# Kernel optimization log

Hardware: AMD Instinct MI355X
Metric: run time of the kernel (lower is better)

The kernel has to match this reference:

```python
import jax, jax.numpy as jnp
import numpy as np

BATCH = 8192
IN_FEATURES = 64
K = 10
OUT_FEATURES = 1000  # classifier assumed fully expanded: t == out_features
SCALING = 1.0
EPS = 1e-12  # F.normalize default eps


def _l2_normalize(v, axis):
    n = jnp.sqrt(jnp.sum(v * v, axis=axis, keepdims=True))
    return v / jnp.maximum(n, EPS)


def setup_inputs() -> dict:
    key = jax.random.key(0)
    k1, k2 = jax.random.split(key)
    x = jax.random.normal(k1, (BATCH, IN_FEATURES), dtype=jnp.float32)
    # kaiming_uniform_(a=sqrt(5)) on (in_features, k, out_features): fan_in = k*out_features
    fan_in = K * OUT_FEATURES
    bound = np.sqrt(6.0 / ((1.0 + 5.0) * fan_in))
    theta = jax.random.uniform(k2, (IN_FEATURES, K, OUT_FEATURES), dtype=jnp.float32,
                               minval=-bound, maxval=bound)
    return {"x": x, "theta": theta}


def reference(x, theta):
    d, k, C = theta.shape
    # theta.permute(0,2,1).reshape(d, C*k).T -> rows are class-major, then proxy index
    th = jnp.transpose(theta, (0, 2, 1)).reshape(d, C * k).T  # (C*k, d)
    th = SCALING * _l2_normalize(th, axis=1)
    a = SCALING * _l2_normalize(x, axis=1)  # (B, d)
    # Only the cross a-theta block of the full pairwise matrix is used downstream;
    # the eye/off-diagonal mask never intersects it (row i < B <= col B+j).
    d2 = (jnp.sum(a * a, axis=1, keepdims=True)
          + jnp.sum(th * th, axis=1)[None, :]
          - 2.0 * (a @ th.T))  # (B, C*k)
    d2 = jnp.maximum(d2, 0.0)
    d2 = jnp.where(d2 > 0.0, d2, 0.0)  # error_mask zeroing (no-op after clamp, kept for fidelity)
    simi = -d2.reshape(x.shape[0], C, k)  # (B, C, k)
    att = jax.nn.softmax(simi, axis=-1)  # gamma = 1
    return jnp.sum(simi * att, axis=-1)  # (B, C)
```

## Files before the change

### kernel.cpp

```cpp
#include <hip/hip_runtime.h>


#define BATCH   8192
#define DIM     64
#define KPROX   10
#define NCLASS  1000
#define NCOL    (NCLASS * KPROX)
#define NBTILE  (BATCH / 16)
#define NNTILE  (NCOL / 16)

#define NBM     32
#define NBN     63
#define XBLKS   (NBTILE / 4)
#define TBLKS   ((NCOL + 255) / 256)

typedef __attribute__((ext_vector_type(8))) short bf16x8;
typedef __attribute__((ext_vector_type(4))) float f32x4;
typedef __attribute__((ext_vector_type(2))) unsigned int u32x2;
typedef __attribute__((ext_vector_type(2))) __fp16 f16x2;
typedef __attribute__((ext_vector_type(4))) __fp16 f16x4;

#define LOG2E 1.4426950408889634f
#define LN2   0.6931471805599453f

__device__ inline unsigned short f32_to_bf16(float f) {
    unsigned int u = __float_as_uint(f);
    u += 0x7FFFu + ((u >> 16) & 1u);
    return (unsigned short)(u >> 16);
}

__device__ inline bf16x8 gload16(const unsigned short* p) {
    bf16x8 r;
    asm volatile("global_load_dwordx4 %0, %1, off" : "=v"(r) : "v"(p));
    return r;
}
__device__ inline float fexp2(float x) {
    float r; asm("v_exp_f32 %0, %1" : "=v"(r) : "v"(x)); return r;
}
#define WAIT_VM(N) do { asm volatile("s_waitcnt vmcnt(" #N ")" ::: "memory"); \
                        __builtin_amdgcn_sched_barrier(0); } while (0)

__global__ __launch_bounds__(256)
void prep_kernel(const float* __restrict__ x, const float* __restrict__ theta,
                 unsigned short* __restrict__ Xf0, unsigned short* __restrict__ Xf1,
                 unsigned short* __restrict__ THf0, unsigned short* __restrict__ THf1) {
    if (blockIdx.x < XBLKS) {
        int wave = threadIdx.x >> 6, lane = threadIdx.x & 63;
        int bt  = blockIdx.x * 4 + wave;
        int r16 = lane & 15, hi = lane >> 4;
        const float* src = x + (size_t)(bt * 16 + r16) * DIM + hi * 8;
        f32x4 v0 = *(const f32x4*)(src);
        f32x4 v1 = *(const f32x4*)(src + 4);
        f32x4 v2 = *(const f32x4*)(src + 32);
        f32x4 v3 = *(const f32x4*)(src + 36);
        float ss = 0.f;
        #pragma unroll
        for (int i = 0; i < 4; ++i)
            ss += v0[i]*v0[i] + v1[i]*v1[i] + v2[i]*v2[i] + v3[i]*v3[i];
        ss += __shfl_xor(ss, 16);
        ss += __shfl_xor(ss, 32);
        float sc = __builtin_amdgcn_rsqf(ss);
        bf16x8 p0, p1;
        #pragma unroll
        for (int i = 0; i < 4; ++i) {
            p0[i]     = (short)f32_to_bf16(v0[i] * sc);
            p0[i + 4] = (short)f32_to_bf16(v1[i] * sc);
            p1[i]     = (short)f32_to_bf16(v2[i] * sc);
            p1[i + 4] = (short)f32_to_bf16(v3[i] * sc);
        }
        ((bf16x8*)Xf0)[bt * 64 + lane] = p0;
        ((bf16x8*)Xf1)[bt * 64 + lane] = p1;
    } else {
        int tid = (blockIdx.x - XBLKS) * 256 + threadIdx.x;
        if (tid >= NCOL) return;
        int kk = tid / NCLASS, c = tid - kk * NCLASS;
        const float* src = theta + kk * NCLASS + c;
        float v[DIM];
        float ss = 0.f;
        #pragma unroll
        for (int d = 0; d < DIM; ++d) {
            v[d] = src[(size_t)d * NCOL];
            ss += v[d] * v[d];
        }
        float sc = __builtin_amdgcn_rsqf(ss);
        int j = c * KPROX + kk;
        int jt = j >> 4, jr = j & 15;
        #pragma unroll
        for (int h = 0; h < 8; ++h) {
            unsigned short* dst = (h < 4 ? THf0 : THf1)
                                + ((size_t)jt * 64 + (h & 3) * 16 + jr) * 8;
            #pragma unroll
            for (int i = 0; i < 8; ++i)
                dst[i] = f32_to_bf16(v[h * 8 + i] * sc);
        }
    }
}

__global__ __launch_bounds__(256, 4)
void podnet_main(const unsigned short* __restrict__ Xf0,
                 const unsigned short* __restrict__ Xf1,
                 const unsigned short* __restrict__ THf0,
                 const unsigned short* __restrict__ THf1,
                 float* __restrict__ out) {
    int bid = blockIdx.x;
    int bm  = bid & 31;
    int bn  = bid >> 5;
    int wave = threadIdx.x >> 6, lane = threadIdx.x & 63;
    int r16 = lane & 15, hi = lane >> 4;

    auto th0 = [&](int ct) {
        int ti = bn * 10 + ct;
        ti = ti > (NNTILE - 1) ? (NNTILE - 1) : ti;
        return THf0 + ((size_t)ti * 64 + lane) * 8;
    };
    auto th1 = [&](int ct) {
        int ti = bn * 10 + ct;
        ti = ti > (NNTILE - 1) ? (NNTILE - 1) : ti;
        return THf1 + ((size_t)ti * 64 + lane) * 8;
    };

    const unsigned short* xp = Xf0 + ((size_t)(bm * 16 + wave * 4) * 64 + lane) * 8;
    const unsigned short* xq = Xf1 + ((size_t)(bm * 16 + wave * 4) * 64 + lane) * 8;
    bf16x8 xa0[4], xa1[4];
    #pragma unroll
    for (int rt = 0; rt < 4; ++rt) {
        xa0[rt] = gload16(xp + (size_t)rt * 64 * 8);
        xa1[rt] = gload16(xq + (size_t)rt * 64 * 8);
    }
    bf16x8 A0 = gload16(th0(0)), A1 = gload16(th1(0));
    bf16x8 B0 = gload16(th0(1)), B1 = gload16(th1(1));

    f32x4 ps[4], ws[4];
    #pragma unroll
    for (int rt = 0; rt < 4; ++rt) {
        ps[rt] = (f32x4){0.f, 0.f, 0.f, 0.f};
        ws[rt] = (f32x4){0.f, 0.f, 0.f, 0.f};
    }

    int target = bn * 16 + r16;
    int Pq     = bn * 160 + hi * 4;

    auto proc = [&](bf16x8 T0, bf16x8 T1, int CT) {
        int P  = Pq + CT * 16;
        int c0 = P / 10;
        int rr = P - c0 * 10;
        bool m0 = (c0 == target);
        bool m1 = (c0 + 1 == target);
        unsigned glo = (m0 ? 0x3C00u : 0u)
                     | ((((rr + 1) < 10) ? m0 : m1) ? 0x3C000000u : 0u);
        unsigned ghi = ((((rr + 2) < 10) ? m0 : m1) ? 0x3C00u : 0u)
                     | ((((rr + 3) < 10) ? m0 : m1) ? 0x3C000000u : 0u);
        u32x2 gu = {glo, ghi};
        f16x4 G = __builtin_bit_cast(f16x4, gu);
        #pragma unroll
        for (int rt = 0; rt < 4; ++rt) {
            f32x4 d = {0.f, 0.f, 0.f, 0.f};
            d = __builtin_amdgcn_mfma_f32_16x16x32_bf16(T0, xa0[rt], d, 0, 0, 0);
            d = __builtin_amdgcn_mfma_f32_16x16x32_bf16(T1, xa1[rt], d, 0, 0, 0);
            float y0 = fminf(fmaf(d[0], 2.f * LOG2E, -2.f * LOG2E), 0.f);
            float y1 = fminf(fmaf(d[1], 2.f * LOG2E, -2.f * LOG2E), 0.f);
            float y2 = fminf(fmaf(d[2], 2.f * LOG2E, -2.f * LOG2E), 0.f);
            float y3 = fminf(fmaf(d[3], 2.f * LOG2E, -2.f * LOG2E), 0.f);
            float e0 = fexp2(y0), e1 = fexp2(y1), e2 = fexp2(y2), e3 = fexp2(y3);
            f16x2 el = __builtin_amdgcn_cvt_pkrtz(e0, e1);
            f16x2 eh = __builtin_amdgcn_cvt_pkrtz(e2, e3);
            f16x2 vl = __builtin_amdgcn_cvt_pkrtz(y0 * e0, y1 * e1);
            f16x2 vh = __builtin_amdgcn_cvt_pkrtz(y2 * e2, y3 * e3);
            f16x4 ef = __builtin_shufflevector(el, eh, 0, 1, 2, 3);
            f16x4 vf = __builtin_shufflevector(vl, vh, 0, 1, 2, 3);
            ps[rt] = __builtin_amdgcn_mfma_f32_16x16x16f16(ef, G, ps[rt], 0, 0, 0);
            ws[rt] = __builtin_amdgcn_mfma_f32_16x16x16f16(vf, G, ws[rt], 0, 0, 0);
        }
    };

    WAIT_VM(2);  proc(A0, A1, 0);  A0 = gload16(th0(2)); A1 = gload16(th1(2));
    WAIT_VM(2);  proc(B0, B1, 1);  B0 = gload16(th0(3)); B1 = gload16(th1(3));
    WAIT_VM(2);  proc(A0, A1, 2);  A0 = gload16(th0(4)); A1 = gload16(th1(4));
    WAIT_VM(2);  proc(B0, B1, 3);  B0 = gload16(th0(5)); B1 = gload16(th1(5));
    WAIT_VM(2);  proc(A0, A1, 4);  A0 = gload16(th0(6)); A1 = gload16(th1(6));
    WAIT_VM(2);  proc(B0, B1, 5);  B0 = gload16(th0(7)); B1 = gload16(th1(7));
    WAIT_VM(2);  proc(A0, A1, 6);  A0 = gload16(th0(8)); A1 = gload16(th1(8));
    WAIT_VM(2);  proc(B0, B1, 7);  B0 = gload16(th0(9)); B1 = gload16(th1(9));
    WAIT_VM(2);  proc(A0, A1, 8);
    WAIT_VM(0);  proc(B0, B1, 9);

    bool ok = target < NCLASS;
    size_t row0 = (size_t)bm * 256 + wave * 64 + hi * 4;
    #pragma unroll
    for (int rt = 0; rt < 4; ++rt) {
        float* op = out + (row0 + rt * 16) * NCLASS + target;
        #pragma unroll
        for (int r = 0; r < 4; ++r) {
            float o = ws[rt][r] * __builtin_amdgcn_rcpf(ps[rt][r]) * LN2;
            if (ok) __builtin_nontemporal_store(o, op + (size_t)r * NCLASS);
        }
    }
}

extern "C" void kernel_launch(void* const* d_in, const int* in_sizes, int n_in,
                              void* d_out, int out_size, void* d_ws, size_t ws_size,
                              hipStream_t stream) {
    const float* x     = (const float*)d_in[0];
    const float* theta = (const float*)d_in[1];
    float* out = (float*)d_out;

    unsigned short* Xf0 = (unsigned short*)d_ws;
    unsigned short* Xf1 = Xf0 + (size_t)NBTILE * 512;
    unsigned short* Tf0 = Xf1 + (size_t)NBTILE * 512;
    unsigned short* Tf1 = Tf0 + (size_t)NNTILE * 512;

    prep_kernel<<<XBLKS + TBLKS, 256, 0, stream>>>(x, theta, Xf0, Xf1, Tf0, Tf1);
    podnet_main<<<NBM * NBN, 256, 0, stream>>>(Xf0, Xf1, Tf0, Tf1, out);
}
```

Before: 38.10 us.

## Move softmax epilogue to packed fp16, simplify mask, remap grid, drop nontemporal stores

Result: faster. 33.82 us (-11.2%).

```diff
diff --git a/kernel.cpp b/kernel.cpp
--- a/kernel.cpp
+++ b/kernel.cpp
@@ -1,4 +1,5 @@
 #include <hip/hip_runtime.h>
+#include <hip/hip_fp16.h>
 
 
 #define BATCH   8192
@@ -17,8 +18,9 @@
 typedef __attribute__((ext_vector_type(8))) short bf16x8;
 typedef __attribute__((ext_vector_type(4))) float f32x4;
 typedef __attribute__((ext_vector_type(2))) unsigned int u32x2;
-typedef __attribute__((ext_vector_type(2))) __fp16 f16x2;
 typedef __attribute__((ext_vector_type(4))) __fp16 f16x4;
+typedef __attribute__((ext_vector_type(2))) _Float16 h16x2;
+typedef __attribute__((ext_vector_type(4))) _Float16 h16x4;
 
 #define LOG2E 1.4426950408889634f
 #define LN2   0.6931471805599453f
@@ -33,9 +35,6 @@
     bf16x8 r;
     asm volatile("global_load_dwordx4 %0, %1, off" : "=v"(r) : "v"(p));
     return r;
-}
-__device__ inline float fexp2(float x) {
-    float r; asm("v_exp_f32 %0, %1" : "=v"(r) : "v"(x)); return r;
 }
 #define WAIT_VM(N) do { asm volatile("s_waitcnt vmcnt(" #N ")" ::: "memory"); \
                         __builtin_amdgcn_sched_barrier(0); } while (0)
@@ -102,9 +101,9 @@
                  const unsigned short* __restrict__ THf0,
                  const unsigned short* __restrict__ THf1,
                  float* __restrict__ out) {
-    int bid = blockIdx.x;
-    int bm  = bid & 31;
-    int bn  = bid >> 5;
+    unsigned bid = blockIdx.x;
+    int bn  = bid % NBN;
+    int bm  = bid / NBN;
     int wave = threadIdx.x >> 6, lane = threadIdx.x & 63;
     int r16 = lane & 15, hi = lane >> 4;
 
@@ -138,18 +137,18 @@
     }
 
     int target = bn * 16 + r16;
-    int Pq     = bn * 160 + hi * 4;
+    int q0     = hi * 4 - 10 * r16;
+
+    const h16x2 K2  = {(_Float16)(2.0f * LOG2E),  (_Float16)(2.0f * LOG2E)};
+    const h16x2 KM2 = {(_Float16)(-2.0f * LOG2E), (_Float16)(-2.0f * LOG2E)};
+    const h16x2 Z2  = {(_Float16)0.0f, (_Float16)0.0f};
 
     auto proc = [&](bf16x8 T0, bf16x8 T1, int CT) {
-        int P  = Pq + CT * 16;
-        int c0 = P / 10;
-        int rr = P - c0 * 10;
-        bool m0 = (c0 == target);
-        bool m1 = (c0 + 1 == target);
-        unsigned glo = (m0 ? 0x3C00u : 0u)
-                     | ((((rr + 1) < 10) ? m0 : m1) ? 0x3C000000u : 0u);
-        unsigned ghi = ((((rr + 2) < 10) ? m0 : m1) ? 0x3C00u : 0u)
-                     | ((((rr + 3) < 10) ? m0 : m1) ? 0x3C000000u : 0u);
+        int q = q0 + CT * 16;
+        unsigned glo = ((unsigned)q       < 10u ? 0x3C00u     : 0u)
+                     | ((unsigned)(q + 1) < 10u ? 0x3C000000u : 0u);
+        unsigned ghi = ((unsigned)(q + 2) < 10u ? 0x3C00u     : 0u)
+                     | ((unsigned)(q + 3) < 10u ? 0x3C000000u : 0u);
         u32x2 gu = {glo, ghi};
         f16x4 G = __builtin_bit_cast(f16x4, gu);
         #pragma unroll
@@ -157,19 +156,20 @@
             f32x4 d = {0.f, 0.f, 0.f, 0.f};
             d = __builtin_amdgcn_mfma_f32_16x16x32_bf16(T0, xa0[rt], d, 0, 0, 0);
             d = __builtin_amdgcn_mfma_f32_16x16x32_bf16(T1, xa1[rt], d, 0, 0, 0);
-            float y0 = fminf(fmaf(d[0], 2.f * LOG2E, -2.f * LOG2E), 0.f);
-            float y1 = fminf(fmaf(d[1], 2.f * LOG2E, -2.f * LOG2E), 0.f);
-            float y2 = fminf(fmaf(d[2], 2.f * LOG2E, -2.f * LOG2E), 0.f);
-            float y3 = fminf(fmaf(d[3], 2.f * LOG2E, -2.f * LOG2E), 0.f);
-            float e0 = fexp2(y0), e1 = fexp2(y1), e2 = fexp2(y2), e3 = fexp2(y3);
-            f16x2 el = __builtin_amdgcn_cvt_pkrtz(e0, e1);
-            f16x2 eh = __builtin_amdgcn_cvt_pkrtz(e2, e3);
-            f16x2 vl = __builtin_amdgcn_cvt_pkrtz(y0 * e0, y1 * e1);
-            f16x2 vh = __builtin_amdgcn_cvt_pkrtz(y2 * e2, y3 * e3);
-            f16x4 ef = __builtin_shufflevector(el, eh, 0, 1, 2, 3);
-            f16x4 vf = __builtin_shufflevector(vl, vh, 0, 1, 2, 3);
-            ps[rt] = __builtin_amdgcn_mfma_f32_16x16x16f16(ef, G, ps[rt], 0, 0, 0);
-            ws[rt] = __builtin_amdgcn_mfma_f32_16x16x16f16(vf, G, ws[rt], 0, 0, 0);
+            h16x2 h01 = __builtin_bit_cast(h16x2, __builtin_amdgcn_cvt_pkrtz(d[0], d[1]));
+            h16x2 h23 = __builtin_bit_cast(h16x2, __builtin_amdgcn_cvt_pkrtz(d[2], d[3]));
+            h16x2 y01 = __builtin_elementwise_min(h16x2(h01 * K2 + KM2), Z2);
+            h16x2 y23 = __builtin_elementwise_min(h16x2(h23 * K2 + KM2), Z2);
+            h16x2 e01 = __builtin_bit_cast(h16x2, h2exp2(__builtin_bit_cast(__half2, y01)));
+            h16x2 e23 = __builtin_bit_cast(h16x2, h2exp2(__builtin_bit_cast(__half2, y23)));
+            h16x2 v01 = y01 * e01;
+            h16x2 v23 = y23 * e23;
+            h16x4 ef4 = __builtin_shufflevector(e01, e23, 0, 1, 2, 3);
+            h16x4 vf4 = __builtin_shufflevector(v01, v23, 0, 1, 2, 3);
+            ps[rt] = __builtin_amdgcn_mfma_f32_16x16x16f16(
+                         __builtin_bit_cast(f16x4, ef4), G, ps[rt], 0, 0, 0);
+            ws[rt] = __builtin_amdgcn_mfma_f32_16x16x16f16(
+                         __builtin_bit_cast(f16x4, vf4), G, ws[rt], 0, 0, 0);
         }
     };
 
@@ -192,7 +192,7 @@
         #pragma unroll
         for (int r = 0; r < 4; ++r) {
             float o = ws[rt][r] * __builtin_amdgcn_rcpf(ps[rt][r]) * LN2;
-            if (ok) __builtin_nontemporal_store(o, op + (size_t)r * NCLASS);
+            if (ok) op[(size_t)r * NCLASS] = o;
         }
     }
 }
```
